# Optimization experiments

Measured on AMD Instinct MI355X. Metric: run time of the kernel, lower is better.

The kernel has to match this reference:

```python
import jax, jax.numpy as jnp
import numpy as np

B, S, DIN, DOUT = 4, 2048, 4096, 4096

def setup_inputs() -> dict:
    key = jax.random.key(0)
    k1, k2, k3, k4 = jax.random.split(key, 4)
    x = jax.random.normal(k1, (B, S, DIN), dtype=jnp.float32)
    # int8-valued weights stored in int32 (harness dtype constraint); values in [-127, 127]
    weight_int8 = jax.random.randint(k2, (DOUT, DIN), -127, 128, dtype=jnp.int32)
    # per-output-channel scales, small positive values typical of int8 quantization
    scale = jax.random.uniform(k3, (DOUT,), dtype=jnp.float32, minval=1e-4, maxval=2e-2)
    bias = jax.random.normal(k4, (DOUT,), dtype=jnp.float32)
    return {"x": x, "weight_int8": weight_int8, "scale": scale, "bias": bias}

def reference(x, weight_int8, scale, bias):
    # Dequantize: w[o, i] = int8[o, i] * scale[o], cast to activation dtype
    w = (weight_int8.astype(jnp.float32) * scale[:, None]).astype(x.dtype)  # [DOUT, DIN]
    # F.linear: y = x @ w.T + bias
    return jnp.einsum('bsi,oi->bso', x, w) + bias
```

## Files before the change

### kernel.cpp

```cpp
#include <hip/hip_runtime.h>
#include <hip/hip_bf16.h>

#define BM 256
#define BN 256
#define BK 64
#define NSLOT 4
#define LDS_BYTES (2 * NSLOT * BM * BK)

typedef float  f32x4  __attribute__((ext_vector_type(4)));
typedef int    i32x4  __attribute__((ext_vector_type(4)));
typedef int    i32x16 __attribute__((ext_vector_type(16)));
typedef __bf16 bf16x8 __attribute__((ext_vector_type(8)));
typedef __bf16 bf16x4 __attribute__((ext_vector_type(4)));

__device__ __forceinline__ void gload_lds16(const void* g, void* l) {
    __builtin_amdgcn_global_load_lds(
        (const __attribute__((address_space(1))) void*)g,
        (__attribute__((address_space(3))) void*)l, 16, 0, 0);
}

__global__ __launch_bounds__(256)
void rowquant_x(const float* __restrict__ x, signed char* __restrict__ xq,
                float* __restrict__ xs, int K) {
    const int row = blockIdx.x;
    const float* xr = x + (size_t)row * K;
    const int tid = threadIdx.x;
    const int n4 = K / 4;

    float mx = 0.f;
    for (int i = tid; i < n4; i += 256) {
        f32x4 v = ((const f32x4*)xr)[i];
        mx = fmaxf(mx, fmaxf(fmaxf(fabsf(v[0]), fabsf(v[1])),
                             fmaxf(fabsf(v[2]), fabsf(v[3]))));
    }
#pragma unroll
    for (int off = 32; off; off >>= 1)
        mx = fmaxf(mx, __shfl_xor(mx, off));
    __shared__ float smx[4];
    if ((tid & 63) == 0) smx[tid >> 6] = mx;
    __syncthreads();
    mx = fmaxf(fmaxf(smx[0], smx[1]), fmaxf(smx[2], smx[3]));

    const float inv = mx > 0.f ? 127.f / mx : 0.f;
    if (tid == 0) xs[row] = mx / 127.f;

    unsigned* out = (unsigned*)(xq + (size_t)row * K);
    for (int i = tid; i < n4; i += 256) {
        f32x4 v = ((const f32x4*)xr)[i];
        int q0 = __float2int_rn(v[0] * inv);
        int q1 = __float2int_rn(v[1] * inv);
        int q2 = __float2int_rn(v[2] * inv);
        int q3 = __float2int_rn(v[3] * inv);
        out[i] = (unsigned)(q0 & 255) | ((unsigned)(q1 & 255) << 8) |
                 ((unsigned)(q2 & 255) << 16) | ((unsigned)(q3 & 255) << 24);
    }
}

__global__ __launch_bounds__(256)
void cvt_w_i8(const int* __restrict__ w, unsigned* __restrict__ wq, int n4) {
    int i = blockIdx.x * 256 + threadIdx.x;
    const int stride = gridDim.x * 256;
    for (; i < n4; i += stride) {
        i32x4 v = ((const i32x4*)w)[i];
        wq[i] = (unsigned)(v[0] & 255) | ((unsigned)(v[1] & 255) << 8) |
                ((unsigned)(v[2] & 255) << 16) | ((unsigned)(v[3] & 255) << 24);
    }
}


__global__ __launch_bounds__(512, 2)
void qlin_gemm_i8(const signed char* __restrict__ A,
                  const signed char* __restrict__ B,
                  const float* __restrict__ xs,
                  const float* __restrict__ scale,
                  const float* __restrict__ bias,
                  float* __restrict__ C, int M, int N, int K) {
    extern __shared__ signed char lds[];
    signed char* lA = lds;
    signed char* lB = lds + NSLOT * (BM * BK);

    const int NTN = N / BN;
    const int nwg = gridDim.x;
    int bid = blockIdx.x;
    bid = (bid & 7) * (nwg >> 3) + (bid >> 3);
    const int tm = bid / NTN;
    const int tn = bid % NTN;

    const int tid  = threadIdx.x;
    const int lane = tid & 63;
    const int wid  = tid >> 6;
    const int wr   = wid >> 2;
    const int wc   = wid & 3;

    const int srow  = wid * 32 + (lane >> 1);
    const int shalf = (lane & 1) ^ ((srow >> 3) & 1);
    const signed char* Abase = A + (size_t)(tm * BM + srow) * K + shalf * 16;
    const signed char* Bbase = B + (size_t)(tn * BN + srow) * K + shalf * 16;

    const int NT = K / BK;

    auto STAGE_A = [&](int t) {
        signed char* d = lA + (t & (NSLOT - 1)) * (BM * BK) + wid * 1024;
#pragma unroll
        for (int j = 0; j < 2; ++j)
            gload_lds16(Abase + t * BK + j * 32, d + j * 8192);
    };
    auto STAGE_B = [&](int t) {
        signed char* d = lB + (t & (NSLOT - 1)) * (BM * BK) + wid * 1024;
#pragma unroll
        for (int j = 0; j < 2; ++j)
            gload_lds16(Bbase + t * BK + j * 32, d + j * 8192);
    };

    const int fr = lane & 31;
    const int fh = lane >> 5;
    const int swz = (fr >> 3) & 1;
    const int ho = ((fh ^ swz) << 4);

    auto READ_A = [&](const signed char* base, int ks, i32x4* fa) {
        const int o = ks * 8192 + ho;
#pragma unroll
        for (int mi = 0; mi < 4; ++mi) {
            const int R = wr * 128 + mi * 32 + fr;
            fa[mi] = *(const i32x4*)(base + R * 32 + o);
        }
    };
    auto READ_B = [&](const signed char* base, int ks, i32x4* fb) {
        const int o = ks * 8192 + ho;
#pragma unroll
        for (int ni = 0; ni < 2; ++ni) {
            const int R = wc * 64 + ni * 32 + fr;
            fb[ni] = *(const i32x4*)(base + R * 32 + o);
        }
    };

    i32x16 acc[4][2];
#pragma unroll
    for (int mi = 0; mi < 4; ++mi)
#pragma unroll
        for (int ni = 0; ni < 2; ++ni)
#pragma unroll
            for (int r = 0; r < 16; ++r) acc[mi][ni][r] = 0;

    for (int u = 0; u < 3 && u < NT; ++u) { STAGE_A(u); STAGE_B(u); }
    {
        const int pre = NT - 1;
        if (pre >= 2)      asm volatile("s_waitcnt vmcnt(8)" ::: "memory");
        else if (pre == 1) asm volatile("s_waitcnt vmcnt(4)" ::: "memory");
        else               asm volatile("s_waitcnt vmcnt(0)" ::: "memory");
    }
    __builtin_amdgcn_s_barrier();

    i32x4 a0[4], b0[2], a1[4], b1[2];
    READ_A(lA, 0, a0); READ_B(lB, 0, b0);

    for (int t = 0; t < NT; ++t) {
        const signed char* lAs = lA + (t & (NSLOT - 1)) * (BM * BK);
        const signed char* lBs = lB + (t & (NSLOT - 1)) * (BM * BK);
        const int rem = NT - 1 - t;

        if (t > 0) {
            if (rem >= 2)      asm volatile("s_waitcnt vmcnt(8)" ::: "memory");
            else if (rem == 1) asm volatile("s_waitcnt vmcnt(4)" ::: "memory");
            else               asm volatile("s_waitcnt vmcnt(0)" ::: "memory");
            __builtin_amdgcn_s_barrier();
        }

        READ_A(lAs, 1, a1); READ_B(lBs, 1, b1);
        if (t + 3 < NT) STAGE_A(t + 3);
        __builtin_amdgcn_s_setprio(1);
#pragma unroll
        for (int mi = 0; mi < 4; ++mi)
#pragma unroll
            for (int ni = 0; ni < 2; ++ni)
                acc[mi][ni] = __builtin_amdgcn_mfma_i32_32x32x32_i8(
                    a0[mi], b0[ni], acc[mi][ni], 0, 0, 0);
        __builtin_amdgcn_s_setprio(0);

        if (rem >= 1) {
            if (rem >= 3)      asm volatile("s_waitcnt vmcnt(6)" ::: "memory");
            else if (rem == 2) asm volatile("s_waitcnt vmcnt(4)" ::: "memory");
            else               asm volatile("s_waitcnt vmcnt(0)" ::: "memory");
            __builtin_amdgcn_s_barrier();

            const signed char* lAn = lA + ((t + 1) & (NSLOT - 1)) * (BM * BK);
            const signed char* lBn = lB + ((t + 1) & (NSLOT - 1)) * (BM * BK);
            READ_A(lAn, 0, a0); READ_B(lBn, 0, b0);
            if (t + 3 < NT) STAGE_B(t + 3);
        }
        __builtin_amdgcn_s_setprio(1);
#pragma unroll
        for (int mi = 0; mi < 4; ++mi)
#pragma unroll
            for (int ni = 0; ni < 2; ++ni)
                acc[mi][ni] = __builtin_amdgcn_mfma_i32_32x32x32_i8(
                    a1[mi], b1[ni], acc[mi][ni], 0, 0, 0);
        __builtin_amdgcn_s_setprio(0);
    }

    const int rb = tm * BM + wr * 128 + 4 * fh;
    const int cb = tn * BN + wc * 64 + fr;
#pragma unroll
    for (int mi = 0; mi < 4; ++mi) {
        float sm[16];
#pragma unroll
        for (int r = 0; r < 16; ++r)
            sm[r] = xs[rb + mi * 32 + (r & 3) + 8 * (r >> 2)];
#pragma unroll
        for (int ni = 0; ni < 2; ++ni) {
            const int n = cb + ni * 32;
            const float sc = scale[n];
            const float bs = bias[n];
#pragma unroll
            for (int r = 0; r < 16; ++r) {
                const int m = rb + mi * 32 + (r & 3) + 8 * (r >> 2);
                C[(size_t)m * N + n] = fmaf((float)acc[mi][ni][r], sm[r] * sc, bs);
            }
        }
    }
}

#define FBM 128
#define FBK 32

__device__ __forceinline__ int swz_elem(int row, int e) {
    return row * FBK + (e ^ (((row >> 1) & 3) << 3));
}

__global__ __launch_bounds__(256, 2)
void qlin_gemm_reg(const float* __restrict__ A, const int* __restrict__ W,
                   const float* __restrict__ scale, const float* __restrict__ bias,
                   float* __restrict__ C, int M, int N, int K) {
    __shared__ __bf16 lA[2][FBM * FBK];
    __shared__ __bf16 lB[2][FBM * FBK];
    const int NTN = N / FBM;
    const int nwg = gridDim.x;
    int bid = blockIdx.x;
    if ((nwg & 7) == 0) bid = (bid & 7) * (nwg >> 3) + (bid >> 3);
    const int tm = bid / NTN, tn = bid % NTN;
    const int tid = threadIdx.x, lane = tid & 63, wid = tid >> 6;
    const int wr = wid >> 1, wc = wid & 1;
    const int srow0 = tid >> 3, skq = tid & 7;
    const float* aptr = A + (size_t)(tm * FBM + srow0) * K + skq * 4;
    const int*   wptr = W + (size_t)(tn * FBM + srow0) * K + skq * 4;
    const size_t rstride = (size_t)32 * K;
    f32x4 sa[4]; i32x4 sw[4];
    auto LOAD = [&](int t) {
#pragma unroll
        for (int j = 0; j < 4; ++j) {
            sa[j] = *(const f32x4*)(aptr + (size_t)t * FBK + j * rstride);
            sw[j] = *(const i32x4*)(wptr + (size_t)t * FBK + j * rstride);
        }
    };
    auto STORE = [&](int buf) {
#pragma unroll
        for (int j = 0; j < 4; ++j) {
            const int idx = swz_elem(srow0 + j * 32, skq * 4);
            bf16x4 va = { (__bf16)sa[j][0], (__bf16)sa[j][1],
                          (__bf16)sa[j][2], (__bf16)sa[j][3] };
            bf16x4 vw = { (__bf16)(float)sw[j][0], (__bf16)(float)sw[j][1],
                          (__bf16)(float)sw[j][2], (__bf16)(float)sw[j][3] };
            *(bf16x4*)&lA[buf][idx] = va;
            *(bf16x4*)&lB[buf][idx] = vw;
        }
    };
    const f32x4 fzero = {0.f, 0.f, 0.f, 0.f};
    f32x4 acc[4][4];
#pragma unroll
    for (int i = 0; i < 4; ++i)
#pragma unroll
        for (int j = 0; j < 4; ++j) acc[i][j] = fzero;
    const int fr = lane & 15, fks = (lane >> 4) * 8;
    LOAD(0); STORE(0); __syncthreads();
    const int NT = K / FBK;
    for (int t = 0; t < NT; ++t) {
        const int buf = t & 1;
        if (t + 1 < NT) LOAD(t + 1);
        bf16x8 af[4], bfg[4];
#pragma unroll
        for (int mi = 0; mi < 4; ++mi)
            af[mi] = *(const bf16x8*)&lA[buf][swz_elem(wr * 64 + mi * 16 + fr, fks)];
#pragma unroll
        for (int ni = 0; ni < 4; ++ni)
            bfg[ni] = *(const bf16x8*)&lB[buf][swz_elem(wc * 64 + ni * 16 + fr, fks)];
#pragma unroll
        for (int mi = 0; mi < 4; ++mi)
#pragma unroll
            for (int ni = 0; ni < 4; ++ni)
                acc[mi][ni] = __builtin_amdgcn_mfma_f32_16x16x32_bf16(
                    af[mi], bfg[ni], acc[mi][ni], 0, 0, 0);
        if (t + 1 < NT) STORE(buf ^ 1);
        __syncthreads();
    }
    const int row0 = tm * FBM + wr * 64 + (lane >> 4) * 4;
    const int col0 = tn * FBM + wc * 64 + fr;
#pragma unroll
    for (int ni = 0; ni < 4; ++ni) {
        const int n = col0 + ni * 16;
        const float sc = scale[n], bs = bias[n];
#pragma unroll
        for (int mi = 0; mi < 4; ++mi) {
            const int m = row0 + mi * 16;
#pragma unroll
            for (int r = 0; r < 4; ++r)
                C[(size_t)(m + r) * N + n] = fmaf(acc[mi][ni][r], sc, bs);
        }
    }
}

extern "C" void kernel_launch(void* const* d_in, const int* in_sizes, int n_in,
                              void* d_out, int out_size, void* d_ws, size_t ws_size,
                              hipStream_t stream) {
    const float* x     = (const float*)d_in[0];
    const int*   w8    = (const int*)d_in[1];
    const float* scale = (const float*)d_in[2];
    const float* bias  = (const float*)d_in[3];
    float*       out   = (float*)d_out;

    const int DOUT = in_sizes[2];
    const int DIN  = in_sizes[1] / DOUT;
    const int M    = in_sizes[0] / DIN;

    const size_t need = (size_t)M * DIN + (size_t)DOUT * DIN + (size_t)M * 4;
    const int nwg = (M / BM) * (DOUT / BN);
    const bool ok = (ws_size >= need) && (M % BM == 0) && (DOUT % BN == 0) &&
                    (DIN % BK == 0) && (nwg % 8 == 0) && (DIN / BK >= 4);
    if (ok) {
        signed char* xq = (signed char*)d_ws;
        signed char* wq = xq + (size_t)M * DIN;
        float*       xs = (float*)(wq + (size_t)DOUT * DIN);
        rowquant_x<<<M, 256, 0, stream>>>(x, xq, xs, DIN);
        cvt_w_i8<<<2048, 256, 0, stream>>>(w8, (unsigned*)wq, DOUT * DIN / 4);
        hipFuncSetAttribute(reinterpret_cast<const void*>(qlin_gemm_i8),
                            hipFuncAttributeMaxDynamicSharedMemorySize, LDS_BYTES);
        qlin_gemm_i8<<<nwg, 512, LDS_BYTES, stream>>>(xq, wq, xs, scale, bias, out,
                                                      M, DOUT, DIN);
    } else {
        dim3 grid((M / FBM) * (DOUT / FBM));
        qlin_gemm_reg<<<grid, 256, 0, stream>>>(x, w8, scale, bias, out, M, DOUT, DIN);
    }
}
```

Baseline: 211.9 us.

## Stagger even and odd waves so LDS reads overlap other waves' MFMA

Restructures the int8 GEMM main loop to one barrier per K-tile, with even and odd waves running different schedules. Even waves read fragments and issue MFMAs in two halves. Odd waves first finish the previous tile's second-half MFMAs, then read both halves, deferring one half to the next iteration. The aim is to stagger LDS traffic against matrix-core use across waves and to drop the second barrier. In exchange, odd waves carry extra fragment registers, and divergent per-wave code paths may complicate scheduling.

```diff
diff --git a/kernel.cpp b/kernel.cpp
--- a/kernel.cpp
+++ b/kernel.cpp
@@ -91,6 +91,7 @@
     const int wid  = tid >> 6;
     const int wr   = wid >> 2;
     const int wc   = wid & 3;
+    const bool odd = (wid & 1) != 0;
 
     const int srow  = wid * 32 + (lane >> 1);
     const int shalf = (lane & 1) ^ ((srow >> 3) & 1);
@@ -142,61 +143,49 @@
 #pragma unroll
             for (int r = 0; r < 16; ++r) acc[mi][ni][r] = 0;
 
+    auto MFMA8 = [&](const i32x4* fa, const i32x4* fb) {
+        __builtin_amdgcn_s_setprio(1);
+#pragma unroll
+        for (int mi = 0; mi < 4; ++mi)
+#pragma unroll
+            for (int ni = 0; ni < 2; ++ni)
+                acc[mi][ni] = __builtin_amdgcn_mfma_i32_32x32x32_i8(
+                    fa[mi], fb[ni], acc[mi][ni], 0, 0, 0);
+        __builtin_amdgcn_s_setprio(0);
+    };
+
     for (int u = 0; u < 3 && u < NT; ++u) { STAGE_A(u); STAGE_B(u); }
-    {
-        const int pre = NT - 1;
-        if (pre >= 2)      asm volatile("s_waitcnt vmcnt(8)" ::: "memory");
-        else if (pre == 1) asm volatile("s_waitcnt vmcnt(4)" ::: "memory");
-        else               asm volatile("s_waitcnt vmcnt(0)" ::: "memory");
-    }
-    __builtin_amdgcn_s_barrier();
 
     i32x4 a0[4], b0[2], a1[4], b1[2];
-    READ_A(lA, 0, a0); READ_B(lB, 0, b0);
 
     for (int t = 0; t < NT; ++t) {
         const signed char* lAs = lA + (t & (NSLOT - 1)) * (BM * BK);
         const signed char* lBs = lB + (t & (NSLOT - 1)) * (BM * BK);
         const int rem = NT - 1 - t;
 
-        if (t > 0) {
-            if (rem >= 2)      asm volatile("s_waitcnt vmcnt(8)" ::: "memory");
-            else if (rem == 1) asm volatile("s_waitcnt vmcnt(4)" ::: "memory");
-            else               asm volatile("s_waitcnt vmcnt(0)" ::: "memory");
-            __builtin_amdgcn_s_barrier();
-        }
-
-        READ_A(lAs, 1, a1); READ_B(lBs, 1, b1);
-        if (t + 3 < NT) STAGE_A(t + 3);
-        __builtin_amdgcn_s_setprio(1);
-#pragma unroll
-        for (int mi = 0; mi < 4; ++mi)
-#pragma unroll
-            for (int ni = 0; ni < 2; ++ni)
-                acc[mi][ni] = __builtin_amdgcn_mfma_i32_32x32x32_i8(
-                    a0[mi], b0[ni], acc[mi][ni], 0, 0, 0);
-        __builtin_amdgcn_s_setprio(0);
-
-        if (rem >= 1) {
-            if (rem >= 3)      asm volatile("s_waitcnt vmcnt(6)" ::: "memory");
-            else if (rem == 2) asm volatile("s_waitcnt vmcnt(4)" ::: "memory");
-            else               asm volatile("s_waitcnt vmcnt(0)" ::: "memory");
-            __builtin_amdgcn_s_barrier();
-
-            const signed char* lAn = lA + ((t + 1) & (NSLOT - 1)) * (BM * BK);
-            const signed char* lBn = lB + ((t + 1) & (NSLOT - 1)) * (BM * BK);
-            READ_A(lAn, 0, a0); READ_B(lBn, 0, b0);
+        asm volatile("s_waitcnt lgkmcnt(0)" ::: "memory");
+        if (rem >= 2)      asm volatile("s_waitcnt vmcnt(8)" ::: "memory");
+        else if (rem == 1) asm volatile("s_waitcnt vmcnt(4)" ::: "memory");
+        else               asm volatile("s_waitcnt vmcnt(0)" ::: "memory");
+        __builtin_amdgcn_s_barrier();
+
+        if (!odd) {
+            READ_A(lAs, 0, a0); READ_B(lBs, 0, b0);
+            if (t + 3 < NT) STAGE_A(t + 3);
+            MFMA8(a0, b0);
+            READ_A(lAs, 1, a0); READ_B(lBs, 1, b0);
             if (t + 3 < NT) STAGE_B(t + 3);
-        }
-        __builtin_amdgcn_s_setprio(1);
-#pragma unroll
-        for (int mi = 0; mi < 4; ++mi)
-#pragma unroll
-            for (int ni = 0; ni < 2; ++ni)
-                acc[mi][ni] = __builtin_amdgcn_mfma_i32_32x32x32_i8(
-                    a1[mi], b1[ni], acc[mi][ni], 0, 0, 0);
-        __builtin_amdgcn_s_setprio(0);
-    }
+            MFMA8(a0, b0);
+        } else {
+            if (t > 0) MFMA8(a1, b1);
+            if (t + 3 < NT) STAGE_A(t + 3);
+            READ_A(lAs, 0, a0); READ_B(lBs, 0, b0);
+            READ_A(lAs, 1, a1); READ_B(lBs, 1, b1);
+            if (t + 3 < NT) STAGE_B(t + 3);
+            MFMA8(a0, b0);
+        }
+    }
+    if (odd) MFMA8(a1, b1);
 
     const int rb = tm * BM + wr * 128 + 4 * fh;
     const int cb = tn * BN + wc * 64 + fr;
```

Result: no change. 209.7 us (-1.0%).
